# Optimization experiments

Measured on AMD Instinct MI355X. Metric: run time of the kernel, lower is better.

The kernel has to match this reference:

```python
import jax, jax.numpy as jnp
import numpy as np

B, S, HID = 2, 2048, 1024
NH = 16
DK = HID // NH


def setup_inputs() -> dict:
    key0 = jax.random.key(0)
    ks = jax.random.split(key0, 16)
    inp = {
        "query": jax.random.normal(ks[0], (B, S, HID), dtype=jnp.float32),
        "key": jax.random.normal(ks[1], (B, S, HID), dtype=jnp.float32),
        "value": jax.random.normal(ks[2], (B, S, HID), dtype=jnp.float32),
        "bias": jax.random.uniform(ks[3], (B, S), dtype=jnp.float32),
        "mask": jax.random.randint(ks[4], (B, 1, S), 0, 2, dtype=jnp.int32),
        "wq": jax.random.normal(ks[5], (HID, HID), dtype=jnp.float32) * 0.02,
        "bq": jax.random.normal(ks[6], (HID,), dtype=jnp.float32) * 0.02,
        "wk": jax.random.normal(ks[7], (HID, HID), dtype=jnp.float32) * 0.02,
        "bk": jax.random.normal(ks[8], (HID,), dtype=jnp.float32) * 0.02,
        "wv": jax.random.normal(ks[9], (HID, HID), dtype=jnp.float32) * 0.02,
        "bv": jax.random.normal(ks[10], (HID,), dtype=jnp.float32) * 0.02,
        "wo": jax.random.normal(ks[11], (HID, HID), dtype=jnp.float32) * 0.02,
        "bo": jax.random.normal(ks[12], (HID,), dtype=jnp.float32) * 0.02,
    }
    return inp


def reference(query, key, value, bias, mask, wq, bq, wk, bk, wv, bv, wo, bo):
    b, s, hid = query.shape
    # attn_bias_type == 'both': gate K and V with per-token scalar bias
    # (dropout is eval-mode identity): x + p[..., None] * x
    key = key + bias[:, :, None] * key
    value = value + bias[:, :, None] * value

    def proj(x, w, bb):
        # torch Linear: x @ W.T + b, then split heads -> [b, nh, s, dk]
        y = x @ w.T + bb
        return y.reshape(b, s, NH, DK).transpose(0, 2, 1, 3)

    q = proj(query, wq, bq)
    k = proj(key, wk, bk)
    v = proj(value, wv, bv)

    scores = jnp.einsum("bhqd,bhkd->bhqk", q, k) / jnp.sqrt(jnp.asarray(DK, q.dtype))
    m = mask[:, None]  # [b,1,1,s] broadcast over heads and query positions
    scores = jnp.where(m == 0, jnp.asarray(-10000.0, scores.dtype), scores)
    p_attn = jax.nn.softmax(scores, axis=-1)
    x = jnp.einsum("bhqk,bhkd->bhqd", p_attn, v)
    x = x.transpose(0, 2, 1, 3).reshape(b, s, hid)
    return x @ wo.T + bo
```

## Files before the change

kernel.cpp:

```cpp
#include <hip/hip_runtime.h>
#include <stdint.h>

#define NB   2
#define SS   2048
#define HIDN 1024
#define NHEAD 16
#define DKK  64

typedef __attribute__((ext_vector_type(8))) short bf16x8;
typedef __attribute__((ext_vector_type(4))) float f32x4;

__device__ __forceinline__ uint16_t f2bf(float f) {
    uint32_t u = __float_as_uint(f);
    u += 0x7FFF + ((u >> 16) & 1);
    return (uint16_t)(u >> 16);
}
__device__ __forceinline__ uint32_t pk2(float f0, float f1) {
    uint32_t u0 = __float_as_uint(f0);
    uint32_t u1 = __float_as_uint(f1);
    u0 += 0x7FFF + ((u0 >> 16) & 1);
    u1 += 0x7FFF + ((u1 >> 16) & 1);
    return (u0 >> 16) | (u1 & 0xFFFF0000u);
}
__device__ __forceinline__ uint32_t cvtpk(float lo, float hi) {
    uint32_t r;
    asm("v_cvt_pk_bf16_f32 %0, %1, %2" : "=v"(r) : "v"(lo), "v"(hi));
    return r;
}
__device__ __forceinline__ float exp2_fast(float x) {
    float r;
    asm("v_exp_f32 %0, %1" : "=v"(r) : "v"(x));
    return r;
}
__device__ __forceinline__ uint4 pack8(const float* __restrict__ s, float sc) {
    float4 a = *(const float4*)s;
    float4 b = *(const float4*)(s + 4);
    uint4 r;
    r.x = pk2(sc * a.x, sc * a.y);
    r.y = pk2(sc * a.z, sc * a.w);
    r.z = pk2(sc * b.x, sc * b.y);
    r.w = pk2(sc * b.z, sc * b.w);
    return r;
}
__device__ __forceinline__ void gl_lds16(const uint16_t* g, uint16_t* l) {
    __builtin_amdgcn_global_load_lds((const __attribute__((address_space(1))) void*)g,
                                     (__attribute__((address_space(3))) void*)l,
                                     16, 0, 0);
}

__global__ __launch_bounds__(256, 4)
void cvt_all(const float* __restrict__ q, const float* __restrict__ k,
             const float* __restrict__ v, const float* __restrict__ bias,
             const float* __restrict__ w0, const float* __restrict__ w1,
             const float* __restrict__ w2, const float* __restrict__ w3,
             uint16_t* __restrict__ q16, uint16_t* __restrict__ k16,
             uint16_t* __restrict__ v16, uint16_t* __restrict__ w16o)
{
    int i = blockIdx.x * 256 + threadIdx.x;
    if (i < 524288) {
        size_t e = (size_t)i * 8;
        float sc = 1.0f + bias[i >> 7];
        *(uint4*)(q16 + e) = pack8(q + e, 1.0f);
        *(uint4*)(k16 + e) = pack8(k + e, sc);
        *(uint4*)(v16 + e) = pack8(v + e, sc);
    } else {
        int j = i - 524288;
        const float* src = (j < 131072) ? w0 : (j < 262144) ? w1
                         : (j < 393216) ? w2 : w3;
        size_t e = (size_t)(j & 131071) * 8;
        *(uint4*)(w16o + (size_t)(j >> 17) * 1048576 + e) = pack8(src + e, 1.0f);
    }
}

__device__ __forceinline__ void gemm_core(const uint16_t* __restrict__ A,
                                          const uint16_t* __restrict__ W,
                                          uint16_t* __restrict__ As,
                                          uint16_t* __restrict__ Bs,
                                          int m0, int n0,
                                          f32x4 acc[4][4])
{
    const int t    = threadIdx.x;
    const int w    = t >> 6;
    const int lane = t & 63;
    const int q    = lane >> 4;
    const int lr   = lane & 15;
    const int wr   = (w >> 1) * 64;
    const int wc   = (w & 1) * 64;
    const int srow = lane >> 3;
    const int sg   = (lane & 7) ^ srow;

    for (int it = 0; it < 16; ++it) {
        const int k0 = it * 64;
#pragma unroll
        for (int c = 0; c < 4; ++c) {
            int r = w * 32 + c * 8;
            gl_lds16(A + (size_t)(m0 + r + srow) * HIDN + k0 + sg * 8,
                     As + r * 64);
            gl_lds16(W + (size_t)(n0 + r + srow) * HIDN + k0 + sg * 8,
                     Bs + r * 64);
        }
        __syncthreads();

        bf16x8 af[2][4], bfr[2][4];
#pragma unroll
        for (int s = 0; s < 2; ++s) {
#pragma unroll
            for (int i = 0; i < 4; ++i)
                af[s][i] = *(const bf16x8*)&As[(wr + i * 16 + lr) * 64 +
                                               (((s * 4 + q) ^ (lr & 7)) * 8)];
#pragma unroll
            for (int j = 0; j < 4; ++j)
                bfr[s][j] = *(const bf16x8*)&Bs[(wc + j * 16 + lr) * 64 +
                                                (((s * 4 + q) ^ (lr & 7)) * 8)];
        }
#pragma unroll
        for (int s = 0; s < 2; ++s)
#pragma unroll
            for (int i = 0; i < 4; ++i)
#pragma unroll
                for (int j = 0; j < 4; ++j)
                    acc[i][j] = __builtin_amdgcn_mfma_f32_16x16x32_bf16(
                        af[s][i], bfr[s][j], acc[i][j], 0, 0, 0);
        __syncthreads();
    }
}

__global__ __launch_bounds__(256, 3)
void gemm_qkv(const uint16_t* __restrict__ Qin, const uint16_t* __restrict__ Kin,
              const uint16_t* __restrict__ Vin, const uint16_t* __restrict__ W16,
              const float* __restrict__ bq, const float* __restrict__ bk,
              const float* __restrict__ bv,
              uint16_t* __restrict__ Qb, uint16_t* __restrict__ Kb,
              uint16_t* __restrict__ Vtb)
{
    __shared__ __align__(16) uint16_t Sh[2 * 128 * 64];
    uint16_t* As = Sh;
    uint16_t* Bs = Sh + 128 * 64;

    const int z = blockIdx.z;
    const uint16_t* A    = (z == 0) ? Qin : (z == 1) ? Kin : Vin;
    const uint16_t* W    = W16 + (size_t)z * 1048576;
    const float*    bias = (z == 0) ? bq : (z == 1) ? bk : bv;
    const float     osc  = (z == 0) ? 0.125f * 1.44269504f : 1.0f;

    const int t    = threadIdx.x;
    const int w    = t >> 6;
    const int lane = t & 63;
    const int q    = lane >> 4;
    const int lr   = lane & 15;
    const int wr   = (w >> 1) * 64;
    const int wc   = (w & 1) * 64;
    const int m0   = blockIdx.y * 128;
    const int n0   = blockIdx.x * 128;

    f32x4 acc[4][4] = {};
    gemm_core(A, W, As, Bs, m0, n0, acc);

    if (z < 2) {
        uint16_t* o = (z == 0) ? Qb : Kb;
#pragma unroll
        for (int i = 0; i < 4; ++i)
#pragma unroll
            for (int j = 0; j < 4; ++j) {
                int gn = n0 + wc + j * 16 + lr;
                float bvx = bias[gn];
#pragma unroll
                for (int r = 0; r < 4; ++r) {
                    int row = m0 + wr + i * 16 + q * 4 + r;
                    int b = row >> 11, s = row & 2047;
                    size_t dst = (size_t)b * (NHEAD * SS * DKK)
                               + (size_t)(gn >> 6) * (SS * DKK)
                               + (size_t)s * DKK + (gn & 63);
                    o[dst] = f2bf((acc[i][j][r] + bvx) * osc);
                }
            }
    } else {
        uint16_t* Tr = Sh;
        int b = m0 >> 11;
#pragma unroll
        for (int hh = 0; hh < 2; ++hh) {
            if ((w & 1) == hh) {
#pragma unroll
                for (int j = 0; j < 4; ++j) {
                    int dl = j * 16 + lr;
                    float bvx = bias[n0 + hh * 64 + dl];
#pragma unroll
                    for (int r = 0; r < 4; ++r) {
                        int sl = wr + (q * 4 + r);
                        Tr[dl * 136 + sl +  0] = f2bf(acc[0][j][r] + bvx);
                        Tr[dl * 136 + sl + 16] = f2bf(acc[1][j][r] + bvx);
                        Tr[dl * 136 + sl + 32] = f2bf(acc[2][j][r] + bvx);
                        Tr[dl * 136 + sl + 48] = f2bf(acc[3][j][r] + bvx);
                    }
                }
            }
            __syncthreads();
            int hgl = (n0 >> 6) + hh;
#pragma unroll
            for (int p = 0; p < 4; ++p) {
                int idx = p * 256 + t;
                int d   = idx >> 4;
                int sc8 = (idx & 15) * 8;
                size_t dst = ((size_t)(b * NHEAD + hgl) * DKK + d) * SS
                           + (m0 & 2047) + sc8;
                *(uint4*)&Vtb[dst] = *(const uint4*)&Tr[d * 136 + sc8];
            }
            __syncthreads();
        }
    }
}

__global__ __launch_bounds__(256, 3)
void gemm_out(const uint16_t* __restrict__ Xb, const uint16_t* __restrict__ W,
              const float* __restrict__ bias, float* __restrict__ out)
{
    __shared__ __align__(16) uint16_t Sh[2 * 128 * 64];
    uint16_t* As = Sh;
    uint16_t* Bs = Sh + 128 * 64;

    const int t    = threadIdx.x;
    const int w    = t >> 6;
    const int lane = t & 63;
    const int q    = lane >> 4;
    const int lr   = lane & 15;
    const int wr   = (w >> 1) * 64;
    const int wc   = (w & 1) * 64;
    const int m0   = blockIdx.y * 128;
    const int n0   = blockIdx.x * 128;

    f32x4 acc[4][4] = {};
    gemm_core(Xb, W, As, Bs, m0, n0, acc);

#pragma unroll
    for (int i = 0; i < 4; ++i)
#pragma unroll
        for (int j = 0; j < 4; ++j) {
            int gn = n0 + wc + j * 16 + lr;
            float bvx = bias[gn];
#pragma unroll
            for (int r = 0; r < 4; ++r) {
                int row = m0 + wr + i * 16 + q * 4 + r;
                out[(size_t)row * HIDN + gn] = acc[i][j][r] + bvx;
            }
        }
}

__global__ __launch_bounds__(512, 4)
void flash_attn(const uint16_t* __restrict__ Qg, const uint16_t* __restrict__ Kg,
                const uint16_t* __restrict__ Vtg, const int* __restrict__ mask,
                uint16_t* __restrict__ X)
{
    __shared__ __align__(16) uint16_t QP[128 * 72];
    __shared__ __align__(16) uint16_t Ks[64 * 72];
    __shared__ __align__(16) uint16_t Vs[64 * 72];
    __shared__ __align__(16) float Amf[SS];

    const int t    = threadIdx.x;
    const int w    = t >> 6;
    const int lane = t & 63;
    const int q    = lane >> 4;
    const int lr   = lane & 15;
    const int bh   = blockIdx.y;
    const int b    = bh >> 4;
    const int h    = bh & 15;
    const int q0   = blockIdx.x * 128;
    const size_t head = (size_t)bh * SS * DKK;

#pragma unroll
    for (int p = 0; p < 2; ++p) {
        int idx = p * 512 + t;
        int row = idx >> 3;
        int col = (idx & 7) * 8;
        *(uint4*)&QP[row * 72 + col] =
            *(const uint4*)(Qg + head + (size_t)(q0 + row) * DKK + col);
    }
#pragma unroll
    for (int p = 0; p < 4; ++p) {
        int i = p * 512 + t;
        Amf[i] = (mask[b * SS + i] == 0) ? -14426.95f : 0.0f;
    }

    const int srow = t >> 3;
    const int scol = (t & 7) * 8;
    uint4 kreg = *(const uint4*)(Kg + head + (size_t)srow * DKK + scol);
    uint4 vreg = *(const uint4*)(Vtg + head + (size_t)srow * SS + scol);

    __syncthreads();

    bf16x8 qf[2];
#pragma unroll
    for (int s = 0; s < 2; ++s)
        qf[s] = *(const bf16x8*)&QP[(w * 16 + lr) * 72 + s * 32 + q * 8];

    float mst = -1e30f, lst = 0.0f;
    f32x4 oacc[4] = {};

    for (int kv0 = 0; kv0 < SS; kv0 += 64) {
        *(uint4*)&Ks[srow * 72 + scol] = kreg;
        *(uint4*)&Vs[srow * 72 + scol] = vreg;
        __syncthreads();

        if (kv0 + 64 < SS) {
            kreg = *(const uint4*)(Kg + head + (size_t)(kv0 + 64 + srow) * DKK + scol);
            vreg = *(const uint4*)(Vtg + head + (size_t)srow * SS + kv0 + 64 + scol);
        }

        f32x4 st[4];
#pragma unroll
        for (int ni = 0; ni < 4; ++ni) {
            bf16x8 kf0 = *(const bf16x8*)&Ks[(ni * 16 + lr) * 72 + 0  + q * 8];
            bf16x8 kf1 = *(const bf16x8*)&Ks[(ni * 16 + lr) * 72 + 32 + q * 8];
            f32x4 z = {0.0f, 0.0f, 0.0f, 0.0f};
            z = __builtin_amdgcn_mfma_f32_16x16x32_bf16(kf0, qf[0], z, 0, 0, 0);
            z = __builtin_amdgcn_mfma_f32_16x16x32_bf16(kf1, qf[1], z, 0, 0, 0);
            st[ni] = z;
        }

        float rmax = -1e30f;
#pragma unroll
        for (int ni = 0; ni < 4; ++ni) {
            float4 am = *(const float4*)&Amf[kv0 + ni * 16 + q * 4];
            st[ni][0] += am.x; st[ni][1] += am.y;
            st[ni][2] += am.z; st[ni][3] += am.w;
#pragma unroll
            for (int r = 0; r < 4; ++r) rmax = fmaxf(rmax, st[ni][r]);
        }
        rmax = fmaxf(rmax, __shfl_xor(rmax, 16));
        rmax = fmaxf(rmax, __shfl_xor(rmax, 32));

        if (__any(rmax > mst + 11.5f)) {
            float mnew  = fmaxf(mst, rmax);
            float alpha = exp2_fast(mst - mnew);
            mst = mnew;
            lst *= alpha;
#pragma unroll
            for (int dj = 0; dj < 4; ++dj) {
                oacc[dj][0] *= alpha; oacc[dj][1] *= alpha;
                oacc[dj][2] *= alpha; oacc[dj][3] *= alpha;
            }
        }

        float rsum = 0.0f;
#pragma unroll
        for (int ni = 0; ni < 4; ++ni) {
            float p0 = exp2_fast(st[ni][0] - mst);
            float p1 = exp2_fast(st[ni][1] - mst);
            float p2 = exp2_fast(st[ni][2] - mst);
            float p3 = exp2_fast(st[ni][3] - mst);
            rsum += (p0 + p1) + (p2 + p3);
            uint2 pw = make_uint2(cvtpk(p0, p1), cvtpk(p2, p3));
            *(uint2*)&QP[(w * 16 + lr) * 72 + ni * 16 + q * 4] = pw;
        }
        rsum += __shfl_xor(rsum, 16);
        rsum += __shfl_xor(rsum, 32);
        lst += rsum;

#pragma unroll
        for (int ks = 0; ks < 2; ++ks) {
            bf16x8 pfB = *(const bf16x8*)&QP[(w * 16 + lr) * 72 + ks * 32 + q * 8];
#pragma unroll
            for (int dj = 0; dj < 4; ++dj) {
                bf16x8 vfA = *(const bf16x8*)&Vs[(dj * 16 + lr) * 72 + ks * 32 + q * 8];
                oacc[dj] = __builtin_amdgcn_mfma_f32_16x16x32_bf16(vfA, pfB, oacc[dj], 0, 0, 0);
            }
        }
        __syncthreads();
    }

    {
        float inv = 1.0f / lst;
        int s = q0 + w * 16 + lr;
        uint16_t* xp = X + (size_t)(b * SS + s) * HIDN + h * DKK;
#pragma unroll
        for (int dj = 0; dj < 4; ++dj) {
            uint2 pw = make_uint2(cvtpk(oacc[dj][0] * inv, oacc[dj][1] * inv),
                                  cvtpk(oacc[dj][2] * inv, oacc[dj][3] * inv));
            *(uint2*)(xp + dj * 16 + q * 4) = pw;
        }
    }
}

extern "C" void kernel_launch(void* const* d_in, const int* in_sizes, int n_in,
                              void* d_out, int out_size, void* d_ws, size_t ws_size,
                              hipStream_t stream) {
    const float* query = (const float*)d_in[0];
    const float* key   = (const float*)d_in[1];
    const float* value = (const float*)d_in[2];
    const float* bias  = (const float*)d_in[3];
    const int*   mask  = (const int*)d_in[4];
    const float* wq = (const float*)d_in[5];
    const float* bq = (const float*)d_in[6];
    const float* wk = (const float*)d_in[7];
    const float* bk = (const float*)d_in[8];
    const float* wv = (const float*)d_in[9];
    const float* bv = (const float*)d_in[10];
    const float* wo = (const float*)d_in[11];
    const float* bo = (const float*)d_in[12];

    const size_t TEN = (size_t)NB * SS * HIDN;
    uint16_t* Qin = (uint16_t*)d_ws;
    uint16_t* Kin = Qin + TEN;
    uint16_t* Vin = Kin + TEN;
    uint16_t* W16 = Vin + TEN;
    uint16_t* Qb  = W16 + 4 * 1048576;
    uint16_t* Kb  = Qb + TEN;
    uint16_t* Vtb = Kb + TEN;
    uint16_t* Xb  = Qin;

    cvt_all<<<4096, 256, 0, stream>>>(query, key, value, bias,
                                      wq, wk, wv, wo, Qin, Kin, Vin, W16);
    gemm_qkv<<<dim3(8, 32, 3), 256, 0, stream>>>(Qin, Kin, Vin, W16,
                                                 bq, bk, bv, Qb, Kb, Vtb);
    flash_attn<<<dim3(SS / 128, NB * NHEAD), 512, 0, stream>>>(Qb, Kb, Vtb, mask, Xb);
    gemm_out<<<dim3(8, 32), 256, 0, stream>>>(Xb, W16 + 3 * 1048576, bo, (float*)d_out);
}
```

Measured before the change: 242.5 us.

## Double-buffer GEMM LDS tiles and XOR-swizzle attention shared memory

The shared GEMM core now ping-pongs between two LDS buffers for A and W, issuing the next k-tile's global-to-LDS loads before computing on the current tile, with one barrier per iteration instead of two. The GEMM kernels drop launch_bounds occupancy from 3 to 2 because LDS per block doubles to 64KB. Separately, the attention kernel replaces padded (72-stride) Q/P/K/V shared layouts with unpadded 64-stride XOR-swizzled layouts to cut LDS footprint and avoid bank conflicts. Risks are lower occupancy in the GEMMs and a possible race on the P buffer if the swizzle mapping is wrong.

Measured after the change: 231.1 us. 4.7% less time.

```diff
diff --git a/kernel.cpp b/kernel.cpp
--- a/kernel.cpp
+++ b/kernel.cpp
@@ -74,8 +74,10 @@
 
 __device__ __forceinline__ void gemm_core(const uint16_t* __restrict__ A,
                                           const uint16_t* __restrict__ W,
-                                          uint16_t* __restrict__ As,
-                                          uint16_t* __restrict__ Bs,
+                                          uint16_t* __restrict__ As0,
+                                          uint16_t* __restrict__ As1,
+                                          uint16_t* __restrict__ Bs0,
+                                          uint16_t* __restrict__ Bs1,
                                           int m0, int n0,
                                           f32x4 acc[4][4])
 {
@@ -89,29 +91,41 @@
     const int srow = lane >> 3;
     const int sg   = (lane & 7) ^ srow;
 
+#pragma unroll
+    for (int c = 0; c < 4; ++c) {
+        int r = w * 32 + c * 8;
+        gl_lds16(A + (size_t)(m0 + r + srow) * HIDN + sg * 8, As0 + r * 64);
+        gl_lds16(W + (size_t)(n0 + r + srow) * HIDN + sg * 8, Bs0 + r * 64);
+    }
+
     for (int it = 0; it < 16; ++it) {
-        const int k0 = it * 64;
-#pragma unroll
-        for (int c = 0; c < 4; ++c) {
-            int r = w * 32 + c * 8;
-            gl_lds16(A + (size_t)(m0 + r + srow) * HIDN + k0 + sg * 8,
-                     As + r * 64);
-            gl_lds16(W + (size_t)(n0 + r + srow) * HIDN + k0 + sg * 8,
-                     Bs + r * 64);
-        }
+        uint16_t* Asc = (it & 1) ? As1 : As0;
+        uint16_t* Bsc = (it & 1) ? Bs1 : Bs0;
+        uint16_t* Asn = (it & 1) ? As0 : As1;
+        uint16_t* Bsn = (it & 1) ? Bs0 : Bs1;
         __syncthreads();
-
+        if (it + 1 < 16) {
+            int k0 = (it + 1) * 64;
+#pragma unroll
+            for (int c = 0; c < 4; ++c) {
+                int r = w * 32 + c * 8;
+                gl_lds16(A + (size_t)(m0 + r + srow) * HIDN + k0 + sg * 8,
+                         Asn + r * 64);
+                gl_lds16(W + (size_t)(n0 + r + srow) * HIDN + k0 + sg * 8,
+                         Bsn + r * 64);
+            }
+        }
         bf16x8 af[2][4], bfr[2][4];
 #pragma unroll
         for (int s = 0; s < 2; ++s) {
 #pragma unroll
             for (int i = 0; i < 4; ++i)
-                af[s][i] = *(const bf16x8*)&As[(wr + i * 16 + lr) * 64 +
-                                               (((s * 4 + q) ^ (lr & 7)) * 8)];
+                af[s][i] = *(const bf16x8*)&Asc[(wr + i * 16 + lr) * 64 +
+                                                (((s * 4 + q) ^ (lr & 7)) * 8)];
 #pragma unroll
             for (int j = 0; j < 4; ++j)
-                bfr[s][j] = *(const bf16x8*)&Bs[(wc + j * 16 + lr) * 64 +
-                                                (((s * 4 + q) ^ (lr & 7)) * 8)];
+                bfr[s][j] = *(const bf16x8*)&Bsc[(wc + j * 16 + lr) * 64 +
+                                                 (((s * 4 + q) ^ (lr & 7)) * 8)];
         }
 #pragma unroll
         for (int s = 0; s < 2; ++s)
@@ -121,11 +135,10 @@
                 for (int j = 0; j < 4; ++j)
                     acc[i][j] = __builtin_amdgcn_mfma_f32_16x16x32_bf16(
                         af[s][i], bfr[s][j], acc[i][j], 0, 0, 0);
-        __syncthreads();
-    }
-}
-
-__global__ __launch_bounds__(256, 3)
+    }
+}
+
+__global__ __launch_bounds__(256, 2)
 void gemm_qkv(const uint16_t* __restrict__ Qin, const uint16_t* __restrict__ Kin,
               const uint16_t* __restrict__ Vin, const uint16_t* __restrict__ W16,
               const float* __restrict__ bq, const float* __restrict__ bk,
@@ -133,9 +146,8 @@
               uint16_t* __restrict__ Qb, uint16_t* __restrict__ Kb,
               uint16_t* __restrict__ Vtb)
 {
-    __shared__ __align__(16) uint16_t Sh[2 * 128 * 64];
-    uint16_t* As = Sh;
-    uint16_t* Bs = Sh + 128 * 64;
+    __shared__ __align__(16) uint16_t As[2][128 * 64];
+    __shared__ __align__(16) uint16_t Bs[2][128 * 64];
 
     const int z = blockIdx.z;
     const uint16_t* A    = (z == 0) ? Qin : (z == 1) ? Kin : Vin;
@@ -154,7 +166,7 @@
     const int n0   = blockIdx.x * 128;
 
     f32x4 acc[4][4] = {};
-    gemm_core(A, W, As, Bs, m0, n0, acc);
+    gemm_core(A, W, As[0], As[1], Bs[0], Bs[1], m0, n0, acc);
 
     if (z < 2) {
         uint16_t* o = (z == 0) ? Qb : Kb;
@@ -175,7 +187,8 @@
                 }
             }
     } else {
-        uint16_t* Tr = Sh;
+        __syncthreads();
+        uint16_t* Tr = As[0];
         int b = m0 >> 11;
 #pragma unroll
         for (int hh = 0; hh < 2; ++hh) {
@@ -210,13 +223,12 @@
     }
 }
 
-__global__ __launch_bounds__(256, 3)
+__global__ __launch_bounds__(256, 2)
 void gemm_out(const uint16_t* __restrict__ Xb, const uint16_t* __restrict__ W,
               const float* __restrict__ bias, float* __restrict__ out)
 {
-    __shared__ __align__(16) uint16_t Sh[2 * 128 * 64];
-    uint16_t* As = Sh;
-    uint16_t* Bs = Sh + 128 * 64;
+    __shared__ __align__(16) uint16_t As[2][128 * 64];
+    __shared__ __align__(16) uint16_t Bs[2][128 * 64];
 
     const int t    = threadIdx.x;
     const int w    = t >> 6;
@@ -229,7 +241,7 @@
     const int n0   = blockIdx.x * 128;
 
     f32x4 acc[4][4] = {};
-    gemm_core(Xb, W, As, Bs, m0, n0, acc);
+    gemm_core(Xb, W, As[0], As[1], Bs[0], Bs[1], m0, n0, acc);
 
 #pragma unroll
     for (int i = 0; i < 4; ++i)
@@ -250,9 +262,9 @@
                 const uint16_t* __restrict__ Vtg, const int* __restrict__ mask,
                 uint16_t* __restrict__ X)
 {
-    __shared__ __align__(16) uint16_t QP[128 * 72];
-    __shared__ __align__(16) uint16_t Ks[64 * 72];
-    __shared__ __align__(16) uint16_t Vs[64 * 72];
+    __shared__ __align__(16) uint16_t QP[128 * 64];
+    __shared__ __align__(16) uint16_t Ks[64 * 64];
+    __shared__ __align__(16) uint16_t Vs[64 * 64];
     __shared__ __align__(16) float Amf[SS];
 
     const int t    = threadIdx.x;
@@ -270,9 +282,9 @@
     for (int p = 0; p < 2; ++p) {
         int idx = p * 512 + t;
         int row = idx >> 3;
-        int col = (idx & 7) * 8;
-        *(uint4*)&QP[row * 72 + col] =
-            *(const uint4*)(Qg + head + (size_t)(q0 + row) * DKK + col);
+        int g   = idx & 7;
+        *(uint4*)&QP[row * 64 + ((g ^ (row & 7)) * 8)] =
+            *(const uint4*)(Qg + head + (size_t)(q0 + row) * DKK + g * 8);
     }
 #pragma unroll
     for (int p = 0; p < 4; ++p) {
@@ -281,7 +293,9 @@
     }
 
     const int srow = t >> 3;
-    const int scol = (t & 7) * 8;
+    const int sgf  = t & 7;
+    const int scol = sgf * 8;
+    const int swz  = (sgf ^ (srow & 7)) * 8;
     uint4 kreg = *(const uint4*)(Kg + head + (size_t)srow * DKK + scol);
     uint4 vreg = *(const uint4*)(Vtg + head + (size_t)srow * SS + scol);
 
@@ -290,14 +304,15 @@
     bf16x8 qf[2];
 #pragma unroll
     for (int s = 0; s < 2; ++s)
-        qf[s] = *(const bf16x8*)&QP[(w * 16 + lr) * 72 + s * 32 + q * 8];
+        qf[s] = *(const bf16x8*)&QP[(w * 16 + lr) * 64 +
+                                    (((s * 4 + q) ^ (lr & 7)) * 8)];
 
     float mst = -1e30f, lst = 0.0f;
     f32x4 oacc[4] = {};
 
     for (int kv0 = 0; kv0 < SS; kv0 += 64) {
-        *(uint4*)&Ks[srow * 72 + scol] = kreg;
-        *(uint4*)&Vs[srow * 72 + scol] = vreg;
+        *(uint4*)&Ks[srow * 64 + swz] = kreg;
+        *(uint4*)&Vs[srow * 64 + swz] = vreg;
         __syncthreads();
 
         if (kv0 + 64 < SS) {
@@ -308,8 +323,10 @@
         f32x4 st[4];
 #pragma unroll
         for (int ni = 0; ni < 4; ++ni) {
-            bf16x8 kf0 = *(const bf16x8*)&Ks[(ni * 16 + lr) * 72 + 0  + q * 8];
-            bf16x8 kf1 = *(const bf16x8*)&Ks[(ni * 16 + lr) * 72 + 32 + q * 8];
+            bf16x8 kf0 = *(const bf16x8*)&Ks[(ni * 16 + lr) * 64 +
+                                             ((q ^ (lr & 7)) * 8)];
+            bf16x8 kf1 = *(const bf16x8*)&Ks[(ni * 16 + lr) * 64 +
+                                             (((4 + q) ^ (lr & 7)) * 8)];
             f32x4 z = {0.0f, 0.0f, 0.0f, 0.0f};
             z = __builtin_amdgcn_mfma_f32_16x16x32_bf16(kf0, qf[0], z, 0, 0, 0);
             z = __builtin_amdgcn_mfma_f32_16x16x32_bf16(kf1, qf[1], z, 0, 0, 0);
@@ -349,7 +366,8 @@
             float p3 = exp2_fast(st[ni][3] - mst);
             rsum += (p0 + p1) + (p2 + p3);
             uint2 pw = make_uint2(cvtpk(p0, p1), cvtpk(p2, p3));
-            *(uint2*)&QP[(w * 16 + lr) * 72 + ni * 16 + q * 4] = pw;
+            *(uint2*)&QP[(w * 16 + lr) * 64 +
+                         (((ni * 2 + (q >> 1)) ^ (lr & 7)) * 8) + (q & 1) * 4] = pw;
         }
         rsum += __shfl_xor(rsum, 16);
         rsum += __shfl_xor(rsum, 32);
@@ -357,10 +375,12 @@
 
 #pragma unroll
         for (int ks = 0; ks < 2; ++ks) {
-            bf16x8 pfB = *(const bf16x8*)&QP[(w * 16 + lr) * 72 + ks * 32 + q * 8];
+            bf16x8 pfB = *(const bf16x8*)&QP[(w * 16 + lr) * 64 +
+                                             (((ks * 4 + q) ^ (lr & 7)) * 8)];
 #pragma unroll
             for (int dj = 0; dj < 4; ++dj) {
-                bf16x8 vfA = *(const bf16x8*)&Vs[(dj * 16 + lr) * 72 + ks * 32 + q * 8];
+                bf16x8 vfA = *(const bf16x8*)&Vs[(dj * 16 + lr) * 64 +
+                                                 (((ks * 4 + q) ^ (lr & 7)) * 8)];
                 oacc[dj] = __builtin_amdgcn_mfma_f32_16x16x32_bf16(vfA, pfB, oacc[dj], 0, 0, 0);
             }
         }
```
